# Optimization experiments

Measured on AMD Instinct MI355X. Metric: run time of the kernel, lower is better.

The kernel has to match this reference:

```python
import jax, jax.numpy as jnp
import numpy as np

B, N, D_IN = 8, 2048, 512
H = 1024          # MLP hidden
D_EMB = 512       # embed output dim
D_ATTN = 256      # attn_layers[-1]; KQ MLP outputs 2*D_ATTN


def setup_inputs() -> dict:
    key = jax.random.key(0)
    ks = jax.random.split(key, 9)
    s = lambda fi, fo: (2.0 / (fi + fo)) ** 0.5
    return {
        "x": jax.random.normal(ks[0], (B, N, D_IN), dtype=jnp.float32),
        # embed MLP: Linear(D_IN,H), ReLU, Linear(H,D_EMB)  (weights stored [in,out])
        "We1": jax.random.normal(ks[1], (D_IN, H), dtype=jnp.float32) * s(D_IN, H),
        "be1": jnp.zeros((H,), dtype=jnp.float32),
        "We2": jax.random.normal(ks[2], (H, D_EMB), dtype=jnp.float32) * s(H, D_EMB),
        "be2": jnp.zeros((D_EMB,), dtype=jnp.float32),
        # KQ MLP: Linear(D_IN,H), ReLU, Linear(H, 2*D_ATTN)
        "Wk1": jax.random.normal(ks[3], (D_IN, H), dtype=jnp.float32) * s(D_IN, H),
        "bk1": jnp.zeros((H,), dtype=jnp.float32),
        "Wk2": jax.random.normal(ks[4], (H, 2 * D_ATTN), dtype=jnp.float32) * s(H, 2 * D_ATTN),
        "bk2": jnp.zeros((2 * D_ATTN,), dtype=jnp.float32),
    }


def reference(x, We1, be1, We2, be2, Wk1, bk1, Wk2, bk2):
    # embed MLP
    embs = jax.nn.relu(x @ We1 + be1) @ We2 + be2            # [B,N,D_EMB]
    # KQ MLP; chunk: first half K, second half Q
    kq = jax.nn.relu(x @ Wk1 + bk1) @ Wk2 + bk2              # [B,N,2*D_ATTN]
    K, Q = kq[..., :D_ATTN], kq[..., D_ATTN:]
    # unscaled attention: softmax(Q K^T) V
    scores = jnp.einsum("bqd,bkd->bqk", Q, K)                # [B,N,N]
    A = jax.nn.softmax(scores, axis=-1)
    return jnp.einsum("bqk,bkd->bqd", A, embs)               # [B,N,D_EMB]
```

## Files before the change

kernel.cpp:

```cpp
#include <hip/hip_runtime.h>
#include <stdint.h>

using fx4   = __attribute__((ext_vector_type(4))) float;
using half8 = __attribute__((ext_vector_type(8))) _Float16;

__device__ __forceinline__ ushort f2h(float x) {
  _Float16 h = (_Float16)x;
  union { _Float16 hv; ushort u; } v; v.hv = h;
  return v.u;
}

__device__ __forceinline__ void gload_lds16(const ushort* g, ushort* l) {
  __builtin_amdgcn_global_load_lds(
      (__attribute__((address_space(1))) const void*)g,
      (__attribute__((address_space(3))) void*)l, 16, 0, 0);
}

#define MFMA16(a, b, c) __builtin_amdgcn_mfma_f32_16x16x32_f16(a, b, c, 0, 0, 0)

__global__ __launch_bounds__(256)
void gemm_bt(const ushort* __restrict__ A, int lda, long long sA,
             const ushort* __restrict__ B, int ldb, long long sB,
             const float* __restrict__ bias,
             void* __restrict__ C, int ldc, long long sC,
             int K, int flags)
{
  __shared__ ushort As[128 * 32];
  __shared__ ushort Bs[128 * 32];
  const int z = blockIdx.z;
  A += (long long)z * sA;
  B += (long long)z * sB;
  const int tid  = threadIdx.x;
  const int lane = tid & 63;
  const int wave = tid >> 6;
  const int wm   = (wave >> 1) * 64;
  const int wn   = (wave & 1) * 64;
  const long long bm = (long long)blockIdx.y * 128;
  const long long bn = (long long)blockIdx.x * 128;

  const int srow = tid >> 2;
  const int skq  = (tid & 3) * 8;
  const ushort* a0 = A + (bm + srow) * lda + skq;
  const ushort* a1 = a0 + 64LL * lda;
  const ushort* b0 = B + (bn + srow) * ldb + skq;
  const ushort* b1 = b0 + 64LL * ldb;
  ushort* lA0 = &As[tid * 8];
  ushort* lA1 = &As[2048 + tid * 8];
  ushort* lB0 = &Bs[tid * 8];
  ushort* lB1 = &Bs[2048 + tid * 8];

  fx4 acc[4][4] = {};
  const ushort* ap = &As[(wm + (lane & 15)) * 32 + (lane >> 4) * 8];
  const ushort* bp = &Bs[(wn + (lane & 15)) * 32 + (lane >> 4) * 8];

  for (int k0 = 0; k0 < K; k0 += 32) {
    gload_lds16(a0, lA0);
    gload_lds16(a1, lA1);
    gload_lds16(b0, lB0);
    gload_lds16(b1, lB1);
    a0 += 32; a1 += 32; b0 += 32; b1 += 32;
    __syncthreads();
    half8 af[4], bv[4];
#pragma unroll
    for (int t = 0; t < 4; ++t) {
      af[t] = *(const half8*)(ap + t * 16 * 32);
      bv[t] = *(const half8*)(bp + t * 16 * 32);
    }
#pragma unroll
    for (int i = 0; i < 4; ++i)
#pragma unroll
      for (int j = 0; j < 4; ++j)
        acc[i][j] = MFMA16(af[i], bv[j], acc[i][j]);
    __syncthreads();
  }

  const int col0 = (int)bn + wn + (lane & 15);
  const int row0 = (int)bm + wm + ((lane >> 4) << 2);

  if (flags & 16) {
    ushort* Ch = (ushort*)C + (long long)z * sC;
#pragma unroll
    for (int j = 0; j < 4; ++j) {
      const int col = col0 + j * 16;
      const float bvv = bias ? bias[col] : 0.0f;
#pragma unroll
      for (int i = 0; i < 4; ++i) {
        const int row = row0 + i * 16;
        ushort4 o;
        o.x = f2h(acc[i][j][0] + bvv);
        o.y = f2h(acc[i][j][1] + bvv);
        o.z = f2h(acc[i][j][2] + bvv);
        o.w = f2h(acc[i][j][3] + bvv);
        *(ushort4*)(Ch + (long long)col * ldc + row) = o;
      }
    }
    return;
  }

  float*  Cf = (float*)C + (long long)z * sC;
  ushort* Ch = (ushort*)C + (long long)z * sC;
#pragma unroll
  for (int j = 0; j < 4; ++j) {
    const int col = col0 + j * 16;
    const float bvv = bias ? bias[col] : 0.0f;
#pragma unroll
    for (int i = 0; i < 4; ++i) {
      const long long row = row0 + i * 16;
#pragma unroll
      for (int r = 0; r < 4; ++r) {
        float v = acc[i][j][r] + bvv;
        if (flags & 1) v = fmaxf(v, 0.0f);
        if (flags & 2) Ch[(row + r) * ldc + col] = f2h(v);
        else           Cf[(row + r) * ldc + col] = v;
      }
    }
  }
}

__global__ __launch_bounds__(512, 2)
void attn_fused(const ushort* __restrict__ KQ, const ushort* __restrict__ EMBT,
                float* __restrict__ out)
{
  __shared__ ushort Qs[20480];
  __shared__ ushort Ps[10240];
  __shared__ float  rmax[256];
  __shared__ float  mstate[64];
  __shared__ float  mnewA[64];
  __shared__ float  alphaA[64];
  __shared__ float  lred[256];

  const int tid  = threadIdx.x;
  const int lane = tid & 63;
  const int w    = tid >> 6;
  const int c    = lane & 15;
  const int q4   = lane >> 4;
  const int qw   = w >> 2;
  const int tw   = w & 3;
  const int dw   = w * 64;
  const int z    = blockIdx.x;
  const long long tb = (long long)z * 2048;
  const int q0   = blockIdx.y * 64;

#pragma unroll
  for (int p = 0; p < 4; ++p) {
    const int cu  = p * 512 + tid;
    const int row = cu >> 5;
    const int kch = cu & 31;
    const int dc  = kch >> 2, qg = kch & 3;
    const half8 v = *(const half8*)(KQ + (tb + q0 + row) * 512 + 256 + dc * 32 + qg * 8);
    *(half8*)(Qs + dc * 2560 + row * 40 + qg * 8) = v;
  }
  if (tid < 64) mstate[tid] = -3.0e38f;
  __syncthreads();

  float l_part[2][4] = {};
  fx4 o[4][4] = {};

  for (int t0 = 0; t0 < 2048; t0 += 128) {
    fx4 s[2][2] = {};
    const ushort* kb0 = KQ + (tb + t0 + tw * 32 + c) * 512;
    const ushort* kb1 = kb0 + 16 * 512;
#pragma unroll
    for (int dc = 0; dc < 8; ++dc) {
      const half8 a0 = *(const half8*)(Qs + dc * 2560 + (qw * 32 + c) * 40 + q4 * 8);
      const half8 a1 = *(const half8*)(Qs + dc * 2560 + (qw * 32 + 16 + c) * 40 + q4 * 8);
      const half8 b0 = *(const half8*)(kb0 + dc * 32 + q4 * 8);
      const half8 b1 = *(const half8*)(kb1 + dc * 32 + q4 * 8);
      s[0][0] = MFMA16(a0, b0, s[0][0]); s[0][1] = MFMA16(a0, b1, s[0][1]);
      s[1][0] = MFMA16(a1, b0, s[1][0]); s[1][1] = MFMA16(a1, b1, s[1][1]);
    }
#pragma unroll
    for (int i = 0; i < 2; ++i) {
      fx4 rm;
#pragma unroll
      for (int r = 0; r < 4; ++r) rm[r] = fmaxf(s[i][0][r], s[i][1][r]);
#pragma unroll
      for (int off = 1; off < 16; off <<= 1)
#pragma unroll
        for (int r = 0; r < 4; ++r) rm[r] = fmaxf(rm[r], __shfl_xor(rm[r], off, 64));
      if (c == 0) {
#pragma unroll
        for (int r = 0; r < 4; ++r)
          rmax[tw * 64 + qw * 32 + i * 16 + q4 * 4 + r] = rm[r];
      }
    }
    __syncthreads();
    if (w == 0) {
      const float mo = mstate[lane];
      float mn = fmaxf(fmaxf(rmax[lane], rmax[64 + lane]),
                       fmaxf(rmax[128 + lane], rmax[192 + lane]));
      mn = fmaxf(mn, mo);
      mnewA[lane]  = mn;
      alphaA[lane] = __expf(mo - mn);
      mstate[lane] = mn;
    }
    __syncthreads();
#pragma unroll
    for (int i = 0; i < 2; ++i)
#pragma unroll
      for (int r = 0; r < 4; ++r) {
        const int q = qw * 32 + i * 16 + q4 * 4 + r;
        const float mn = mnewA[q];
        const float e0 = __expf(s[i][0][r] - mn);
        const float e1 = __expf(s[i][1][r] - mn);
        l_part[i][r] = alphaA[q] * l_part[i][r] + e0 + e1;
        Ps[tw * 2560 + q * 40 + c]      = f2h(e0);
        Ps[tw * 2560 + q * 40 + 16 + c] = f2h(e1);
      }
#pragma unroll
    for (int i4 = 0; i4 < 4; ++i4)
#pragma unroll
      for (int r = 0; r < 4; ++r) {
        const float aq = alphaA[i4 * 16 + q4 * 4 + r];
#pragma unroll
        for (int n = 0; n < 4; ++n) o[i4][n][r] *= aq;
      }
    __syncthreads();
#pragma unroll
    for (int kc = 0; kc < 4; ++kc) {
      half8 vb[4];
#pragma unroll
      for (int n = 0; n < 4; ++n)
        vb[n] = *(const half8*)(EMBT + (long long)(dw + n * 16 + c) * 16384 +
                                tb + t0 + kc * 32 + q4 * 8);
      half8 pa[4];
#pragma unroll
      for (int i4 = 0; i4 < 4; ++i4)
        pa[i4] = *(const half8*)(Ps + kc * 2560 + (i4 * 16 + c) * 40 + q4 * 8);
#pragma unroll
      for (int i4 = 0; i4 < 4; ++i4)
#pragma unroll
        for (int n = 0; n < 4; ++n)
          o[i4][n] = MFMA16(pa[i4], vb[n], o[i4][n]);
    }
  }

#pragma unroll
  for (int i = 0; i < 2; ++i) {
    fx4 lv;
#pragma unroll
    for (int r = 0; r < 4; ++r) lv[r] = l_part[i][r];
#pragma unroll
    for (int off = 1; off < 16; off <<= 1)
#pragma unroll
      for (int r = 0; r < 4; ++r) lv[r] += __shfl_xor(lv[r], off, 64);
    if (c == 0) {
#pragma unroll
      for (int r = 0; r < 4; ++r)
        lred[tw * 64 + qw * 32 + i * 16 + q4 * 4 + r] = lv[r];
    }
  }
  __syncthreads();
  if (w == 0)
    alphaA[lane] = 1.0f / (lred[lane] + lred[64 + lane] + lred[128 + lane] + lred[192 + lane]);
  __syncthreads();

  float* ob = out + (tb + q0) * 512 + dw;
#pragma unroll
  for (int i4 = 0; i4 < 4; ++i4)
#pragma unroll
    for (int r = 0; r < 4; ++r) {
      const int q = i4 * 16 + q4 * 4 + r;
      const float li = alphaA[q];
#pragma unroll
      for (int n = 0; n < 4; ++n)
        ob[(long long)q * 512 + n * 16 + c] = o[i4][n][r] * li;
    }
}

__global__ __launch_bounds__(256)
void transpose_cast_w(const float* __restrict__ in, ushort* __restrict__ out, int R, int C) {
  __shared__ float tile[32][33];
  const int c0 = blockIdx.x * 32, r0 = blockIdx.y * 32;
  const int tx = threadIdx.x & 31, ty = threadIdx.x >> 5;
#pragma unroll
  for (int i = 0; i < 32; i += 8)
    tile[ty + i][tx] = in[(long long)(r0 + ty + i) * C + (c0 + tx)];
  __syncthreads();
#pragma unroll
  for (int i = 0; i < 32; i += 8)
    out[(long long)(c0 + ty + i) * R + (r0 + tx)] = f2h(tile[tx][ty + i]);
}

__global__ __launch_bounds__(256)
void cast_f32_f16(const float* __restrict__ in, ushort* __restrict__ out) {
  const long long i = ((long long)blockIdx.x * 256 + threadIdx.x) * 4;
  const float4 v = *(const float4*)(in + i);
  ushort4 o;
  o.x = f2h(v.x); o.y = f2h(v.y); o.z = f2h(v.z); o.w = f2h(v.w);
  *(ushort4*)(out + i) = o;
}

__global__ __launch_bounds__(256)
void concat_bias(const float* __restrict__ b0, const float* __restrict__ b1,
                 float* __restrict__ out) {
  const int i = blockIdx.x * 256 + threadIdx.x;
  out[i] = (i < 1024) ? b0[i] : b1[i - 1024];
}

extern "C" void kernel_launch(void* const* d_in, const int* in_sizes, int n_in,
                              void* d_out, int out_size, void* d_ws, size_t ws_size,
                              hipStream_t stream) {
  (void)in_sizes; (void)n_in; (void)out_size; (void)ws_size;
  const float* x   = (const float*)d_in[0];
  const float* We1 = (const float*)d_in[1];
  const float* be1 = (const float*)d_in[2];
  const float* We2 = (const float*)d_in[3];
  const float* be2 = (const float*)d_in[4];
  const float* Wk1 = (const float*)d_in[5];
  const float* bk1 = (const float*)d_in[6];
  const float* Wk2 = (const float*)d_in[7];
  const float* bk2 = (const float*)d_in[8];
  float* out = (float*)d_out;
  char* ws = (char*)d_ws;

  ushort* Xb   = (ushort*)(ws + 0);
  ushort* W2c  = (ushort*)(ws + 0);
  ushort* H    = (ushort*)(ws + 16777216);
  ushort* EMBT = (ushort*)(ws + 83886080);
  ushort* KQ   = (ushort*)(ws + 100663296);
  float*  b1c  = (float*)(ws + 117440512);
  ushort* W1c  = (ushort*)(ws + 117448704);

  cast_f32_f16<<<dim3(8192), 256, 0, stream>>>(x, Xb);
  transpose_cast_w<<<dim3(32, 16), 256, 0, stream>>>(We1, W1c, 512, 1024);
  transpose_cast_w<<<dim3(32, 16), 256, 0, stream>>>(Wk1, W1c + 524288, 512, 1024);
  concat_bias<<<dim3(8), 256, 0, stream>>>(be1, bk1, b1c);

  gemm_bt<<<dim3(16, 128, 1), 256, 0, stream>>>(Xb, 512, 0, W1c, 512, 0, b1c,
                                                H, 2048, 0, 512, 1 | 2);

  transpose_cast_w<<<dim3(16, 32), 256, 0, stream>>>(We2, W2c, 1024, 512);
  transpose_cast_w<<<dim3(16, 32), 256, 0, stream>>>(Wk2, W2c + 524288, 1024, 512);

  gemm_bt<<<dim3(4, 128, 1), 256, 0, stream>>>(H, 2048, 0, W2c, 1024, 0, be2,
                                               EMBT, 16384, 0, 1024, 16);
  gemm_bt<<<dim3(4, 128, 1), 256, 0, stream>>>(H + 1024, 2048, 0, W2c + 524288, 1024, 0, bk2,
                                               KQ, 512, 0, 1024, 2);

  attn_fused<<<dim3(8, 32), 512, 0, stream>>>(KQ, EMBT, out);
}
```

Before: 390.8 us.

## Merge paired launches and prefetch K/V tiles into registers in attention

The two transpose-cast launches per layer are merged into one launch with a z dimension. The two second-layer GEMMs become a single launch that picks its problem by blockIdx.z. This cuts launch count and lets both GEMMs fill the GPU together (512 → 1024 blocks). In the attention kernel, all K fragments for a tile are loaded up front, and the V (EMBT) fragments are loaded before the softmax phase so their latency overlaps with the reductions and barriers. This raises register pressure in a kernel with launch bounds (512,2).

```diff
diff --git a/kernel.cpp b/kernel.cpp
--- a/kernel.cpp
+++ b/kernel.cpp
@@ -18,25 +18,21 @@
 
 #define MFMA16(a, b, c) __builtin_amdgcn_mfma_f32_16x16x32_f16(a, b, c, 0, 0, 0)
 
-__global__ __launch_bounds__(256)
-void gemm_bt(const ushort* __restrict__ A, int lda, long long sA,
-             const ushort* __restrict__ B, int ldb, long long sB,
-             const float* __restrict__ bias,
-             void* __restrict__ C, int ldc, long long sC,
-             int K, int flags)
+__device__ __forceinline__ void gemm_body(
+    const ushort* __restrict__ A, int lda,
+    const ushort* __restrict__ B, int ldb,
+    const float* __restrict__ bias,
+    void* __restrict__ C, int ldc,
+    int K, int flags, int bx, int by,
+    ushort* As, ushort* Bs)
 {
-  __shared__ ushort As[128 * 32];
-  __shared__ ushort Bs[128 * 32];
-  const int z = blockIdx.z;
-  A += (long long)z * sA;
-  B += (long long)z * sB;
   const int tid  = threadIdx.x;
   const int lane = tid & 63;
   const int wave = tid >> 6;
   const int wm   = (wave >> 1) * 64;
   const int wn   = (wave & 1) * 64;
-  const long long bm = (long long)blockIdx.y * 128;
-  const long long bn = (long long)blockIdx.x * 128;
+  const long long bm = (long long)by * 128;
+  const long long bn = (long long)bx * 128;
 
   const int srow = tid >> 2;
   const int skq  = (tid & 3) * 8;
@@ -78,7 +74,7 @@
   const int row0 = (int)bm + wm + ((lane >> 4) << 2);
 
   if (flags & 16) {
-    ushort* Ch = (ushort*)C + (long long)z * sC;
+    ushort* Ch = (ushort*)C;
 #pragma unroll
     for (int j = 0; j < 4; ++j) {
       const int col = col0 + j * 16;
@@ -97,8 +93,8 @@
     return;
   }
 
-  float*  Cf = (float*)C + (long long)z * sC;
-  ushort* Ch = (ushort*)C + (long long)z * sC;
+  float*  Cf = (float*)C;
+  ushort* Ch = (ushort*)C;
 #pragma unroll
   for (int j = 0; j < 4; ++j) {
     const int col = col0 + j * 16;
@@ -115,6 +111,37 @@
       }
     }
   }
+}
+
+__global__ __launch_bounds__(256)
+void gemm_bt(const ushort* __restrict__ A, int lda, long long sA,
+             const ushort* __restrict__ B, int ldb, long long sB,
+             const float* __restrict__ bias,
+             void* __restrict__ C, int ldc, long long sC,
+             int K, int flags)
+{
+  __shared__ ushort As[128 * 32];
+  __shared__ ushort Bs[128 * 32];
+  const int z = blockIdx.z;
+  void* Cz = (flags & (2 | 16)) ? (void*)((ushort*)C + (long long)z * sC)
+                                : (void*)((float*)C + (long long)z * sC);
+  gemm_body(A + (long long)z * sA, lda, B + (long long)z * sB, ldb, bias,
+            Cz, ldc, K, flags, blockIdx.x, blockIdx.y, As, Bs);
+}
+
+__global__ __launch_bounds__(256)
+void gemm2_pair(const ushort* __restrict__ H, const ushort* __restrict__ W2c,
+                const float* __restrict__ be2, const float* __restrict__ bk2,
+                ushort* __restrict__ EMBT, ushort* __restrict__ KQ)
+{
+  __shared__ ushort As[128 * 32];
+  __shared__ ushort Bs[128 * 32];
+  if (blockIdx.z == 0)
+    gemm_body(H, 2048, W2c, 1024, be2, EMBT, 16384, 1024, 16,
+              blockIdx.x, blockIdx.y, As, Bs);
+  else
+    gemm_body(H + 1024, 2048, W2c + 524288, 1024, bk2, KQ, 512, 1024, 2,
+              blockIdx.x, blockIdx.y, As, Bs);
 }
 
 __global__ __launch_bounds__(512, 2)
@@ -157,18 +184,29 @@
   fx4 o[4][4] = {};
 
   for (int t0 = 0; t0 < 2048; t0 += 128) {
-    fx4 s[2][2] = {};
+    half8 kb[2][8];
     const ushort* kb0 = KQ + (tb + t0 + tw * 32 + c) * 512;
     const ushort* kb1 = kb0 + 16 * 512;
+#pragma unroll
+    for (int dc = 0; dc < 8; ++dc) {
+      kb[0][dc] = *(const half8*)(kb0 + dc * 32 + q4 * 8);
+      kb[1][dc] = *(const half8*)(kb1 + dc * 32 + q4 * 8);
+    }
+    fx4 s[2][2] = {};
 #pragma unroll
     for (int dc = 0; dc < 8; ++dc) {
       const half8 a0 = *(const half8*)(Qs + dc * 2560 + (qw * 32 + c) * 40 + q4 * 8);
       const half8 a1 = *(const half8*)(Qs + dc * 2560 + (qw * 32 + 16 + c) * 40 + q4 * 8);
-      const half8 b0 = *(const half8*)(kb0 + dc * 32 + q4 * 8);
-      const half8 b1 = *(const half8*)(kb1 + dc * 32 + q4 * 8);
-      s[0][0] = MFMA16(a0, b0, s[0][0]); s[0][1] = MFMA16(a0, b1, s[0][1]);
-      s[1][0] = MFMA16(a1, b0, s[1][0]); s[1][1] = MFMA16(a1, b1, s[1][1]);
-    }
+      s[0][0] = MFMA16(a0, kb[0][dc], s[0][0]); s[0][1] = MFMA16(a0, kb[1][dc], s[0][1]);
+      s[1][0] = MFMA16(a1, kb[0][dc], s[1][0]); s[1][1] = MFMA16(a1, kb[1][dc], s[1][1]);
+    }
+    half8 vb[4][4];
+#pragma unroll
+    for (int kc = 0; kc < 4; ++kc)
+#pragma unroll
+      for (int n = 0; n < 4; ++n)
+        vb[kc][n] = *(const half8*)(EMBT + (long long)(dw + n * 16 + c) * 16384 +
+                                    tb + t0 + kc * 32 + q4 * 8);
 #pragma unroll
     for (int i = 0; i < 2; ++i) {
       fx4 rm;
@@ -218,11 +256,6 @@
     __syncthreads();
 #pragma unroll
     for (int kc = 0; kc < 4; ++kc) {
-      half8 vb[4];
-#pragma unroll
-      for (int n = 0; n < 4; ++n)
-        vb[n] = *(const half8*)(EMBT + (long long)(dw + n * 16 + c) * 16384 +
-                                tb + t0 + kc * 32 + q4 * 8);
       half8 pa[4];
 #pragma unroll
       for (int i4 = 0; i4 < 4; ++i4)
@@ -231,7 +264,7 @@
       for (int i4 = 0; i4 < 4; ++i4)
 #pragma unroll
         for (int n = 0; n < 4; ++n)
-          o[i4][n] = MFMA16(pa[i4], vb[n], o[i4][n]);
+          o[i4][n] = MFMA16(pa[i4], vb[kc][n], o[i4][n]);
     }
   }
 
@@ -269,8 +302,12 @@
 }
 
 __global__ __launch_bounds__(256)
-void transpose_cast_w(const float* __restrict__ in, ushort* __restrict__ out, int R, int C) {
+void transpose_cast_w2(const float* __restrict__ in0, const float* __restrict__ in1,
+                       ushort* __restrict__ out0, ushort* __restrict__ out1,
+                       int R, int C) {
   __shared__ float tile[32][33];
+  const float* in  = blockIdx.z ? in1 : in0;
+  ushort*      outp = blockIdx.z ? out1 : out0;
   const int c0 = blockIdx.x * 32, r0 = blockIdx.y * 32;
   const int tx = threadIdx.x & 31, ty = threadIdx.x >> 5;
 #pragma unroll
@@ -279,7 +316,7 @@
   __syncthreads();
 #pragma unroll
   for (int i = 0; i < 32; i += 8)
-    out[(long long)(c0 + ty + i) * R + (r0 + tx)] = f2h(tile[tx][ty + i]);
+    outp[(long long)(c0 + ty + i) * R + (r0 + tx)] = f2h(tile[tx][ty + i]);
 }
 
 __global__ __launch_bounds__(256)
@@ -323,20 +360,15 @@
   ushort* W1c  = (ushort*)(ws + 117448704);
 
   cast_f32_f16<<<dim3(8192), 256, 0, stream>>>(x, Xb);
-  transpose_cast_w<<<dim3(32, 16), 256, 0, stream>>>(We1, W1c, 512, 1024);
-  transpose_cast_w<<<dim3(32, 16), 256, 0, stream>>>(Wk1, W1c + 524288, 512, 1024);
+  transpose_cast_w2<<<dim3(32, 16, 2), 256, 0, stream>>>(We1, Wk1, W1c, W1c + 524288, 512, 1024);
   concat_bias<<<dim3(8), 256, 0, stream>>>(be1, bk1, b1c);
 
   gemm_bt<<<dim3(16, 128, 1), 256, 0, stream>>>(Xb, 512, 0, W1c, 512, 0, b1c,
                                                 H, 2048, 0, 512, 1 | 2);
 
-  transpose_cast_w<<<dim3(16, 32), 256, 0, stream>>>(We2, W2c, 1024, 512);
-  transpose_cast_w<<<dim3(16, 32), 256, 0, stream>>>(Wk2, W2c + 524288, 1024, 512);
-
-  gemm_bt<<<dim3(4, 128, 1), 256, 0, stream>>>(H, 2048, 0, W2c, 1024, 0, be2,
-                                               EMBT, 16384, 0, 1024, 16);
-  gemm_bt<<<dim3(4, 128, 1), 256, 0, stream>>>(H + 1024, 2048, 0, W2c + 524288, 1024, 0, bk2,
-                                               KQ, 512, 0, 1024, 2);
+  transpose_cast_w2<<<dim3(16, 32, 2), 256, 0, stream>>>(We2, Wk2, W2c, W2c + 524288, 1024, 512);
+
+  gemm2_pair<<<dim3(4, 128, 2), 256, 0, stream>>>(H, W2c, be2, bk2, EMBT, KQ);
 
   attn_fused<<<dim3(8, 32), 512, 0, stream>>>(KQ, EMBT, out);
 }
```

After: 353.9 us. 1.1x faster.
